# Optimization experiments

Hardware: AMD Instinct MI355X
Metric: run time of the kernel (lower is better)

Reference implementation:

```python
import jax, jax.numpy as jnp
import numpy as np


def setup_inputs() -> dict:
    key = jax.random.key(0)
    ks = jax.random.split(key, 6)
    B, S, E, H = 8, 2048, 1024, 64
    scale = 1.0 / np.sqrt(E)
    return {
        "query": jax.random.normal(ks[0], (B, S, E), dtype=jnp.float32),
        "key": jax.random.normal(ks[1], (B, S, E), dtype=jnp.float32),
        "value": jax.random.normal(ks[2], (B, S, E), dtype=jnp.float32),
        "Wq": jax.random.normal(ks[3], (E, H), dtype=jnp.float32) * scale,
        "bq": jnp.zeros((H,), dtype=jnp.float32),
        "Wk": jax.random.normal(ks[4], (E, H), dtype=jnp.float32) * scale,
        "bk": jnp.zeros((H,), dtype=jnp.float32),
        "Wv": jax.random.normal(ks[5], (E, H), dtype=jnp.float32) * scale,
        "bv": jnp.zeros((H,), dtype=jnp.float32),
    }


def reference(query, key, value, Wq, bq, Wk, bk, Wv, bv):
    # Linear projections: [B,S,E] @ [E,H] + [H] -> [B,S,H]
    q = jnp.einsum("bse,eh->bsh", query, Wq) + bq
    k = jnp.einsum("bse,eh->bsh", key, Wk) + bk
    v = jnp.einsum("bse,eh->bsh", value, Wv) + bv
    head_dim = q.shape[-1]
    # scores [B,S,S], softmax over last axis, then weighted sum of values
    scores = jnp.einsum("bqh,bkh->bqk", q, k) / jnp.sqrt(
        jnp.asarray(head_dim, dtype=q.dtype)
    )
    attn = jax.nn.softmax(scores, axis=-1)
    return jnp.einsum("bqk,bkh->bqh", attn, v)
```

## Files before the change

### kernel.cpp

```cpp
#include <hip/hip_runtime.h>
#include <math.h>

#define BB 8
#define SS 2048
#define EE 1024
#define HH 64
#define MM (BB * SS)

typedef unsigned short u16;
typedef __attribute__((ext_vector_type(8))) short short8;
typedef __attribute__((ext_vector_type(4))) float floatx4;

__device__ __forceinline__ u16 f2bf(float f) {
    union { float f; unsigned u; } a; a.f = f;
    unsigned r = a.u + 0x7fffu + ((a.u >> 16) & 1u);
    return (u16)(r >> 16);
}

__device__ __forceinline__ void split2(float f0, float f1, unsigned& hp, unsigned& lp) {
    union { float f; unsigned u; } a0, a1, h0, h1, l0, l1;
    a0.f = f0; a1.f = f1;
    h0.u = a0.u & 0xffff0000u;
    h1.u = a1.u & 0xffff0000u;
    l0.f = f0 - h0.f;
    l1.f = f1 - h1.f;
    hp = __builtin_amdgcn_perm(a1.u, a0.u, 0x07060302u);
    lp = __builtin_amdgcn_perm(l1.u, l0.u, 0x07060302u);
}

#define BMROWS 64
#define NCHUNK (EE / 64)

__device__ __forceinline__ void stage_w(const float4* wv, int wk, int wn,
                                        u16 (*__restrict__ wh)[72],
                                        u16 (*__restrict__ wl)[72]) {
    #pragma unroll
    for (int j = 0; j < 4; ++j) {
        const float e0 = (&wv[0].x)[j], e1 = (&wv[1].x)[j],
                    e2 = (&wv[2].x)[j], e3 = (&wv[3].x)[j];
        unsigned hp0, lp0, hp1, lp1;
        split2(e0, e1, hp0, lp0);
        split2(e2, e3, hp1, lp1);
        uint2 h2 = {hp0, hp1};
        uint2 l2 = {lp0, lp1};
        *(uint2*)&wh[wn + j][wk] = h2;
        *(uint2*)&wl[wn + j][wk] = l2;
    }
}

__global__ __launch_bounds__(256) void proj_mfma(
    const float* __restrict__ A0, const float* __restrict__ A1, const float* __restrict__ A2,
    const float* __restrict__ W0, const float* __restrict__ W1, const float* __restrict__ W2,
    const float* __restrict__ b0, const float* __restrict__ b1, const float* __restrict__ b2,
    u16* __restrict__ o0, u16* __restrict__ o1, u16* __restrict__ o2)
{
    const int which = blockIdx.y;
    const float* __restrict__ A    = (which == 0) ? A0 : (which == 1) ? A1 : A2;
    const float* __restrict__ W    = (which == 0) ? W0 : (which == 1) ? W1 : W2;
    const float* __restrict__ bias = (which == 0) ? b0 : (which == 1) ? b1 : b2;
    u16* __restrict__ out          = (which == 0) ? o0 : (which == 1) ? o1 : o2;

    __shared__ __align__(16) u16 Wh[2][64][72], Wl[2][64][72];

    const int tid  = threadIdx.x;
    const int lane = tid & 63;
    const int wave = tid >> 6;
    const int n    = lane & 15;
    const int g    = lane >> 4;
    const int row0 = blockIdx.x * BMROWS;

    const float* __restrict__ ap = A + (size_t)(row0 + wave * 16 + n) * EE + g * 8;

    const int wk = (tid >> 4) * 4;
    const int wn = (tid & 15) * 4;

    floatx4 acc[4];
    #pragma unroll
    for (int nt = 0; nt < 4; ++nt) acc[nt] = (floatx4){0.f, 0.f, 0.f, 0.f};

    float4 wv[4];
    #pragma unroll
    for (int i = 0; i < 4; ++i)
        wv[i] = *(const float4*)&W[(size_t)(wk + i) * HH + wn];

    float4 av[4];
    av[0] = *(const float4*)(ap + 0);
    av[1] = *(const float4*)(ap + 4);
    av[2] = *(const float4*)(ap + 32);
    av[3] = *(const float4*)(ap + 36);

    stage_w(wv, wk, wn, Wh[0], Wl[0]);
    __syncthreads();

    for (int t = 0; t < NCHUNK; ++t) {
        const int cur = t & 1;

        float4 ac[4];
        #pragma unroll
        for (int i = 0; i < 4; ++i) ac[i] = av[i];

        if (t + 1 < NCHUNK) {
            const float* apn = ap + (t + 1) * 64;
            av[0] = *(const float4*)(apn + 0);
            av[1] = *(const float4*)(apn + 4);
            av[2] = *(const float4*)(apn + 32);
            av[3] = *(const float4*)(apn + 36);
            #pragma unroll
            for (int i = 0; i < 4; ++i)
                wv[i] = *(const float4*)&W[(size_t)((t + 1) * 64 + wk + i) * HH + wn];
        }

        #pragma unroll
        for (int ks = 0; ks < 2; ++ks) {
            unsigned hp0, lp0, hp1, lp1, hp2, lp2, hp3, lp3;
            split2(ac[ks * 2].x,     ac[ks * 2].y,     hp0, lp0);
            split2(ac[ks * 2].z,     ac[ks * 2].w,     hp1, lp1);
            split2(ac[ks * 2 + 1].x, ac[ks * 2 + 1].y, hp2, lp2);
            split2(ac[ks * 2 + 1].z, ac[ks * 2 + 1].w, hp3, lp3);
            union { uint4 u; short8 s; } ch, cl;
            ch.u = (uint4){hp0, hp1, hp2, hp3};
            cl.u = (uint4){lp0, lp1, lp2, lp3};
            const short8 ah = ch.s, al = cl.s;

            #pragma unroll
            for (int nt = 0; nt < 4; ++nt) {
                const short8 whf = *(const short8*)&Wh[cur][nt * 16 + n][ks * 32 + g * 8];
                const short8 wlf = *(const short8*)&Wl[cur][nt * 16 + n][ks * 32 + g * 8];
                acc[nt] = __builtin_amdgcn_mfma_f32_16x16x32_bf16(ah, whf, acc[nt], 0, 0, 0);
                acc[nt] = __builtin_amdgcn_mfma_f32_16x16x32_bf16(al, whf, acc[nt], 0, 0, 0);
                acc[nt] = __builtin_amdgcn_mfma_f32_16x16x32_bf16(ah, wlf, acc[nt], 0, 0, 0);
            }
        }

        if (t + 1 < NCHUNK)
            stage_w(wv, wk, wn, Wh[cur ^ 1], Wl[cur ^ 1]);
        __syncthreads();
    }

    #pragma unroll
    for (int nt = 0; nt < 4; ++nt) {
        const float bv = bias[nt * 16 + n];
        #pragma unroll
        for (int r = 0; r < 4; ++r) {
            const int row = row0 + wave * 16 + g * 4 + r;
            out[(size_t)row * HH + nt * 16 + n] = f2bf(acc[nt][r] + bv);
        }
    }
}

__global__ __launch_bounds__(256) void flash_mfma(
    const u16* __restrict__ qp, const u16* __restrict__ kp,
    const u16* __restrict__ vp, float* __restrict__ out)
{
    __shared__ __align__(16) u16 Ks[2][64 * 64];
    __shared__ __align__(16) u16 Vt[2][64 * 64];
    __shared__ __align__(16) u16 Pw[4][16 * 72];

    const int b    = blockIdx.y;
    const int q0   = blockIdx.x * 32;
    const int tid  = threadIdx.x;
    const int lane = tid & 63;
    const int wave = tid >> 6;
    const int wq   = wave & 1;
    const int ks   = wave >> 1;
    const int n    = lane & 15;
    const int g    = lane >> 4;

    const u16* qrow = qp + ((size_t)b * SS + q0 + wq * 16 + n) * HH;
    const short8 qa0 = *(const short8*)(qrow + g * 8);
    const short8 qa1 = *(const short8*)(qrow + 32 + g * 8);

    floatx4 Oa[4];
    #pragma unroll
    for (int ht = 0; ht < 4; ++ht) Oa[ht] = (floatx4){0.f, 0.f, 0.f, 0.f};
    float m_i[4], l_i[4];
    #pragma unroll
    for (int r = 0; r < 4; ++r) { m_i[r] = -1e30f; l_i[r] = 0.f; }

    const u16* kb = kp + (size_t)b * SS * HH;
    const u16* vb = vp + (size_t)b * SS * HH;

    const int jK0 = tid >> 3, jK1 = 32 + (tid >> 3), cs = tid & 7;
    const int jV  = (tid & 15) * 4, hV = (tid >> 4) * 4;

    short8  kr0, kr1;
    ushort4 vr0, vr1, vr2, vr3;

    kr0 = *(const short8*)(kb + (size_t)jK0 * HH + cs * 8);
    kr1 = *(const short8*)(kb + (size_t)jK1 * HH + cs * 8);
    vr0 = *(const ushort4*)(vb + (size_t)(jV + 0) * HH + hV);
    vr1 = *(const ushort4*)(vb + (size_t)(jV + 1) * HH + hV);
    vr2 = *(const ushort4*)(vb + (size_t)(jV + 2) * HH + hV);
    vr3 = *(const ushort4*)(vb + (size_t)(jV + 3) * HH + hV);
    {
        *(short8*)&Ks[0][jK0 * 64 + ((cs ^ (jK0 & 7)) << 3)] = kr0;
        *(short8*)&Ks[0][jK1 * 64 + ((cs ^ (jK1 & 7)) << 3)] = kr1;
        const u16* a0 = (const u16*)&vr0; const u16* a1 = (const u16*)&vr1;
        const u16* a2 = (const u16*)&vr2; const u16* a3 = (const u16*)&vr3;
        #pragma unroll
        for (int i = 0; i < 4; ++i) {
            const int h = hV + i;
            ushort4 w; w.x = a0[i]; w.y = a1[i]; w.z = a2[i]; w.w = a3[i];
            *(ushort4*)((char*)&Vt[0][0] + h * 128 + (((jV >> 3) ^ (h & 7)) << 4) + ((jV & 4) << 1)) = w;
        }
    }
    __syncthreads();

    for (int t = 0; t < SS / 64; ++t) {
        const int cur = t & 1;

        if (t + 1 < SS / 64) {
            const size_t kt = (size_t)(t + 1) * 64;
            kr0 = *(const short8*)(kb + (kt + jK0) * HH + cs * 8);
            kr1 = *(const short8*)(kb + (kt + jK1) * HH + cs * 8);
            vr0 = *(const ushort4*)(vb + (kt + jV + 0) * HH + hV);
            vr1 = *(const ushort4*)(vb + (kt + jV + 1) * HH + hV);
            vr2 = *(const ushort4*)(vb + (kt + jV + 2) * HH + hV);
            vr3 = *(const ushort4*)(vb + (kt + jV + 3) * HH + hV);
        }

        floatx4 S[2];
        #pragma unroll
        for (int nt = 0; nt < 2; ++nt) {
            const int j = ks * 32 + nt * 16 + n;
            const short8 kf0 = *(const short8*)&Ks[cur][j * 64 + (((0 + g) ^ (j & 7)) << 3)];
            const short8 kf1 = *(const short8*)&Ks[cur][j * 64 + (((4 + g) ^ (j & 7)) << 3)];
            floatx4 a = (floatx4){0.f, 0.f, 0.f, 0.f};
            a = __builtin_amdgcn_mfma_f32_16x16x32_bf16(qa0, kf0, a, 0, 0, 0);
            a = __builtin_amdgcn_mfma_f32_16x16x32_bf16(qa1, kf1, a, 0, 0, 0);
            S[nt] = a;
        }

        float mx[4];
        #pragma unroll
        for (int r = 0; r < 4; ++r) mx[r] = -1e30f;
        #pragma unroll
        for (int nt = 0; nt < 2; ++nt)
            #pragma unroll
            for (int r = 0; r < 4; ++r) {
                S[nt][r] *= 0.125f;
                mx[r] = fmaxf(mx[r], S[nt][r]);
            }
        #pragma unroll
        for (int off = 8; off >= 1; off >>= 1)
            #pragma unroll
            for (int r = 0; r < 4; ++r)
                mx[r] = fmaxf(mx[r], __shfl_xor(mx[r], off, 64));

        float alpha[4], ps[4];
        #pragma unroll
        for (int r = 0; r < 4; ++r) {
            const float Mn = fmaxf(m_i[r], mx[r]);
            alpha[r] = __expf(m_i[r] - Mn);
            m_i[r]   = Mn;
            ps[r]    = 0.f;
        }
        float p[2][4];
        #pragma unroll
        for (int nt = 0; nt < 2; ++nt)
            #pragma unroll
            for (int r = 0; r < 4; ++r) {
                p[nt][r] = __expf(S[nt][r] - m_i[r]);
                ps[r] += p[nt][r];
            }
        #pragma unroll
        for (int off = 8; off >= 1; off >>= 1)
            #pragma unroll
            for (int r = 0; r < 4; ++r)
                ps[r] += __shfl_xor(ps[r], off, 64);
        #pragma unroll
        for (int r = 0; r < 4; ++r) l_i[r] = l_i[r] * alpha[r] + ps[r];
        #pragma unroll
        for (int ht = 0; ht < 4; ++ht)
            #pragma unroll
            for (int r = 0; r < 4; ++r) Oa[ht][r] *= alpha[r];

        #pragma unroll
        for (int nt = 0; nt < 2; ++nt)
            #pragma unroll
            for (int r = 0; r < 4; ++r)
                Pw[wave][(g * 4 + r) * 72 + nt * 16 + n] = f2bf(p[nt][r]);
        const short8 pa = *(const short8*)&Pw[wave][n * 72 + g * 8];

        #pragma unroll
        for (int ht = 0; ht < 4; ++ht) {
            const int h = ht * 16 + n;
            const short8 vf = *(const short8*)((const char*)&Vt[cur][0] + h * 128 +
                                               ((((ks << 2) + g) ^ (h & 7)) << 4));
            Oa[ht] = __builtin_amdgcn_mfma_f32_16x16x32_bf16(pa, vf, Oa[ht], 0, 0, 0);
        }

        if (t + 1 < SS / 64) {
            const int nx = cur ^ 1;
            *(short8*)&Ks[nx][jK0 * 64 + ((cs ^ (jK0 & 7)) << 3)] = kr0;
            *(short8*)&Ks[nx][jK1 * 64 + ((cs ^ (jK1 & 7)) << 3)] = kr1;
            const u16* a0 = (const u16*)&vr0; const u16* a1 = (const u16*)&vr1;
            const u16* a2 = (const u16*)&vr2; const u16* a3 = (const u16*)&vr3;
            #pragma unroll
            for (int i = 0; i < 4; ++i) {
                const int h = hV + i;
                ushort4 w; w.x = a0[i]; w.y = a1[i]; w.z = a2[i]; w.w = a3[i];
                *(ushort4*)((char*)&Vt[nx][0] + h * 128 + (((jV >> 3) ^ (h & 7)) << 4) + ((jV & 4) << 1)) = w;
            }
        }
        __syncthreads();
    }

    float* Cb = (float*)&Ks[0][0];
    float* Cm = Cb + 2 * 16 * 68;
    float* Cl = Cm + 32;
    if (ks == 1) {
        #pragma unroll
        for (int ht = 0; ht < 4; ++ht)
            #pragma unroll
            for (int r = 0; r < 4; ++r)
                Cb[(wq * 16 + g * 4 + r) * 68 + ht * 16 + n] = Oa[ht][r];
        if (n == 0)
            #pragma unroll
            for (int r = 0; r < 4; ++r) {
                Cm[wq * 16 + g * 4 + r] = m_i[r];
                Cl[wq * 16 + g * 4 + r] = l_i[r];
            }
    }
    __syncthreads();
    if (ks == 0) {
        float a0v[4], a1v[4], linv[4];
        #pragma unroll
        for (int r = 0; r < 4; ++r) {
            const int m = g * 4 + r;
            const float m1 = Cm[wq * 16 + m], l1 = Cl[wq * 16 + m];
            const float M  = fmaxf(m_i[r], m1);
            const float e0 = __expf(m_i[r] - M), e1 = __expf(m1 - M);
            a0v[r] = e0; a1v[r] = e1;
            linv[r] = 1.f / (l_i[r] * e0 + l1 * e1);
        }
        #pragma unroll
        for (int ht = 0; ht < 4; ++ht)
            #pragma unroll
            for (int r = 0; r < 4; ++r) {
                const float o1 = Cb[(wq * 16 + g * 4 + r) * 68 + ht * 16 + n];
                const float v  = (Oa[ht][r] * a0v[r] + o1 * a1v[r]) * linv[r];
                out[((size_t)b * SS + q0 + wq * 16 + g * 4 + r) * HH + ht * 16 + n] = v;
            }
    }
}

extern "C" void kernel_launch(void* const* d_in, const int* in_sizes, int n_in,
                              void* d_out, int out_size, void* d_ws, size_t ws_size,
                              hipStream_t stream) {
    const float* query = (const float*)d_in[0];
    const float* key   = (const float*)d_in[1];
    const float* value = (const float*)d_in[2];
    const float* Wq    = (const float*)d_in[3];
    const float* bq    = (const float*)d_in[4];
    const float* Wk    = (const float*)d_in[5];
    const float* bk    = (const float*)d_in[6];
    const float* Wv    = (const float*)d_in[7];
    const float* bv    = (const float*)d_in[8];
    float* out = (float*)d_out;

    u16* qp = (u16*)d_ws;
    u16* kp = qp + (size_t)MM * HH;
    u16* vp = kp + (size_t)MM * HH;

    dim3 pgrid(MM / BMROWS, 3);
    proj_mfma<<<pgrid, 256, 0, stream>>>(query, key, value,
                                         Wq, Wk, Wv,
                                         bq, bk, bv,
                                         qp, kp, vp);

    dim3 agrid(SS / 32, BB);
    flash_mfma<<<agrid, 256, 0, stream>>>(qp, kp, vp, out);
}
```

Baseline: 274.7 us.

## Prepack projection weights into MFMA fragment layout and drop LDS staging

Adds a small pre-kernel that splits each weight matrix into bf16 hi/lo parts and stores them in the exact per-lane MFMA fragment order in workspace. The projection kernel then loads weight fragments straight from global memory (L2-resident, shared across blocks) instead of converting and staging them through LDS with per-chunk barriers. This removes the redundant per-block weight conversion, the LDS traffic and the __syncthreads. In exchange it adds a kernel launch and global/L2 loads of the fragments inside the MFMA loop, without explicit prefetch.

```diff
diff --git a/kernel.cpp b/kernel.cpp
--- a/kernel.cpp
+++ b/kernel.cpp
@@ -28,39 +28,52 @@
     lp = __builtin_amdgcn_perm(l1.u, l0.u, 0x07060302u);
 }
 
+#define WP_MAT 131072
+
+__global__ __launch_bounds__(512) void pack_w(
+    const float* __restrict__ W0, const float* __restrict__ W1, const float* __restrict__ W2,
+    u16* __restrict__ Wp)
+{
+    const int which = blockIdx.y;
+    const float* __restrict__ W = (which == 0) ? W0 : (which == 1) ? W1 : W2;
+    const int t    = blockIdx.x;
+    const int tid  = threadIdx.x;
+    const int ks   = tid >> 8;
+    const int nt   = (tid >> 6) & 3;
+    const int lane = tid & 63;
+    const int n    = lane & 15;
+    const int g    = lane >> 4;
+
+    const int k0 = t * 64 + ks * 32 + g * 8;
+    const int c  = nt * 16 + n;
+
+    float e[8];
+    #pragma unroll
+    for (int j = 0; j < 8; ++j) e[j] = W[(size_t)(k0 + j) * HH + c];
+
+    unsigned hp[4], lp[4];
+    #pragma unroll
+    for (int i = 0; i < 4; ++i) split2(e[2 * i], e[2 * i + 1], hp[i], lp[i]);
+
+    u16* dst = Wp + (size_t)which * WP_MAT
+                  + ((size_t)(t * 8 + ks * 4 + nt) * 2) * 512 + lane * 8;
+    *(uint4*)dst         = (uint4){hp[0], hp[1], hp[2], hp[3]};
+    *(uint4*)(dst + 512) = (uint4){lp[0], lp[1], lp[2], lp[3]};
+}
+
 #define BMROWS 64
 #define NCHUNK (EE / 64)
 
-__device__ __forceinline__ void stage_w(const float4* wv, int wk, int wn,
-                                        u16 (*__restrict__ wh)[72],
-                                        u16 (*__restrict__ wl)[72]) {
-    #pragma unroll
-    for (int j = 0; j < 4; ++j) {
-        const float e0 = (&wv[0].x)[j], e1 = (&wv[1].x)[j],
-                    e2 = (&wv[2].x)[j], e3 = (&wv[3].x)[j];
-        unsigned hp0, lp0, hp1, lp1;
-        split2(e0, e1, hp0, lp0);
-        split2(e2, e3, hp1, lp1);
-        uint2 h2 = {hp0, hp1};
-        uint2 l2 = {lp0, lp1};
-        *(uint2*)&wh[wn + j][wk] = h2;
-        *(uint2*)&wl[wn + j][wk] = l2;
-    }
-}
-
 __global__ __launch_bounds__(256) void proj_mfma(
     const float* __restrict__ A0, const float* __restrict__ A1, const float* __restrict__ A2,
-    const float* __restrict__ W0, const float* __restrict__ W1, const float* __restrict__ W2,
+    const u16* __restrict__ Wp,
     const float* __restrict__ b0, const float* __restrict__ b1, const float* __restrict__ b2,
     u16* __restrict__ o0, u16* __restrict__ o1, u16* __restrict__ o2)
 {
     const int which = blockIdx.y;
     const float* __restrict__ A    = (which == 0) ? A0 : (which == 1) ? A1 : A2;
-    const float* __restrict__ W    = (which == 0) ? W0 : (which == 1) ? W1 : W2;
     const float* __restrict__ bias = (which == 0) ? b0 : (which == 1) ? b1 : b2;
     u16* __restrict__ out          = (which == 0) ? o0 : (which == 1) ? o1 : o2;
-
-    __shared__ __align__(16) u16 Wh[2][64][72], Wl[2][64][72];
 
     const int tid  = threadIdx.x;
     const int lane = tid & 63;
@@ -70,18 +83,11 @@
     const int row0 = blockIdx.x * BMROWS;
 
     const float* __restrict__ ap = A + (size_t)(row0 + wave * 16 + n) * EE + g * 8;
-
-    const int wk = (tid >> 4) * 4;
-    const int wn = (tid & 15) * 4;
+    const u16* __restrict__ wpb = Wp + (size_t)which * WP_MAT + lane * 8;
 
     floatx4 acc[4];
     #pragma unroll
     for (int nt = 0; nt < 4; ++nt) acc[nt] = (floatx4){0.f, 0.f, 0.f, 0.f};
-
-    float4 wv[4];
-    #pragma unroll
-    for (int i = 0; i < 4; ++i)
-        wv[i] = *(const float4*)&W[(size_t)(wk + i) * HH + wn];
 
     float4 av[4];
     av[0] = *(const float4*)(ap + 0);
@@ -89,12 +95,7 @@
     av[2] = *(const float4*)(ap + 32);
     av[3] = *(const float4*)(ap + 36);
 
-    stage_w(wv, wk, wn, Wh[0], Wl[0]);
-    __syncthreads();
-
     for (int t = 0; t < NCHUNK; ++t) {
-        const int cur = t & 1;
-
         float4 ac[4];
         #pragma unroll
         for (int i = 0; i < 4; ++i) ac[i] = av[i];
@@ -105,10 +106,9 @@
             av[1] = *(const float4*)(apn + 4);
             av[2] = *(const float4*)(apn + 32);
             av[3] = *(const float4*)(apn + 36);
-            #pragma unroll
-            for (int i = 0; i < 4; ++i)
-                wv[i] = *(const float4*)&W[(size_t)((t + 1) * 64 + wk + i) * HH + wn];
-        }
+        }
+
+        const u16* wpc = wpb + (size_t)t * 8192;
 
         #pragma unroll
         for (int ks = 0; ks < 2; ++ks) {
@@ -124,17 +124,13 @@
 
             #pragma unroll
             for (int nt = 0; nt < 4; ++nt) {
-                const short8 whf = *(const short8*)&Wh[cur][nt * 16 + n][ks * 32 + g * 8];
-                const short8 wlf = *(const short8*)&Wl[cur][nt * 16 + n][ks * 32 + g * 8];
+                const short8 whf = *(const short8*)(wpc + ((ks * 4 + nt) * 2 + 0) * 512);
+                const short8 wlf = *(const short8*)(wpc + ((ks * 4 + nt) * 2 + 1) * 512);
                 acc[nt] = __builtin_amdgcn_mfma_f32_16x16x32_bf16(ah, whf, acc[nt], 0, 0, 0);
                 acc[nt] = __builtin_amdgcn_mfma_f32_16x16x32_bf16(al, whf, acc[nt], 0, 0, 0);
                 acc[nt] = __builtin_amdgcn_mfma_f32_16x16x32_bf16(ah, wlf, acc[nt], 0, 0, 0);
             }
         }
-
-        if (t + 1 < NCHUNK)
-            stage_w(wv, wk, wn, Wh[cur ^ 1], Wl[cur ^ 1]);
-        __syncthreads();
     }
 
     #pragma unroll
@@ -362,10 +358,14 @@
     u16* qp = (u16*)d_ws;
     u16* kp = qp + (size_t)MM * HH;
     u16* vp = kp + (size_t)MM * HH;
+    u16* Wp = vp + (size_t)MM * HH;
+
+    dim3 wgrid(NCHUNK, 3);
+    pack_w<<<wgrid, 512, 0, stream>>>(Wq, Wk, Wv, Wp);
 
     dim3 pgrid(MM / BMROWS, 3);
     proj_mfma<<<pgrid, 256, 0, stream>>>(query, key, value,
-                                         Wq, Wk, Wv,
+                                         Wp,
                                          bq, bk, bv,
                                          qp, kp, vp);
 
```

After: 290.5 us. 5.7% more time.
